# Kernel tuning notes

Hardware: AMD Instinct MI355X
Metric: run time of the kernel (lower is better)

Reference implementation:

```python
import jax, jax.numpy as jnp
import numpy as np

IN_FEATURES = 4096
OUT_FEATURES = 4096
BLOCK_SIZE = 64
P = 0.1          # fraction of blocks kept
N_TOKENS = 8192


def setup_inputs() -> dict:
    key = jax.random.key(0)
    k_x, k_w, k_m, k_b = jax.random.split(key, 4)
    x = jax.random.normal(k_x, (N_TOKENS, IN_FEATURES), dtype=jnp.float32)
    # kaiming_uniform_(a=sqrt(5)) on [out, in] -> bound = 1/sqrt(in_features)
    bound = 1.0 / np.sqrt(IN_FEATURES)
    weight = jax.random.uniform(k_w, (OUT_FEATURES, IN_FEATURES), dtype=jnp.float32,
                                minval=-bound, maxval=bound)
    bias = jax.random.uniform(k_b, (OUT_FEATURES,), dtype=jnp.float32,
                              minval=-bound, maxval=bound)
    # Block-structured 0/1 mask: keep each BLOCK_SIZE x BLOCK_SIZE block with prob P
    nb_out, nb_in = OUT_FEATURES // BLOCK_SIZE, IN_FEATURES // BLOCK_SIZE
    block_keep = (jax.random.uniform(k_m, (nb_out, nb_in)) < P).astype(jnp.float32)
    mask = jnp.repeat(jnp.repeat(block_keep, BLOCK_SIZE, axis=0), BLOCK_SIZE, axis=1)
    return {"input": x, "weight": weight, "bias": bias, "mask": mask}


def reference(input, weight, bias, mask):
    # bsr_dense_mm((W*mask).to_sparse_bsr(), x.T).T + bias == x @ (W*mask).T + bias
    masked_w = weight * mask                      # [out, in]
    return input @ masked_w.T + bias              # [N, out]
```

## Files before the change

kernel.cpp:

```cpp
#include <hip/hip_runtime.h>
#include <hip/hip_fp16.h>
#include <cstdint>

#define IN_F   4096
#define OUT_F  4096
#define BS     64
#define NB     64
#define N_TOK  8192
#define TM     256
#define NMT    (N_TOK / TM)

typedef __attribute__((ext_vector_type(8))) _Float16       f16x8;
typedef __attribute__((ext_vector_type(8))) unsigned short u16x8;
typedef __attribute__((ext_vector_type(4))) unsigned short u16x4;
typedef __attribute__((ext_vector_type(4))) float          f32x4;

#define WS_XT_OFF      0ull
#define WS_XT_BYTES    (2048ull * 32768ull)
#define WS_WT_OFF      (WS_XT_OFF + WS_XT_BYTES)
#define WS_WT_BYTES    (4096ull * 8192ull)
#define WS_NEEDED      (WS_WT_OFF + WS_WT_BYTES)

__device__ __forceinline__ unsigned long long mask_ballot(
        const float* __restrict__ mask, int br, int lane) {
    float mv = mask[(size_t)(br * BS) * IN_F + (size_t)lane * BS];
    return __ballot(mv != 0.0f);
}

__device__ __forceinline__ u16x8 pack8(f32x4 a, f32x4 b) {
    u16x8 o;
#pragma unroll
    for (int j = 0; j < 4; ++j) o[j]     = __half_as_ushort(__float2half_rn(a[j]));
#pragma unroll
    for (int j = 0; j < 4; ++j) o[4 + j] = __half_as_ushort(__float2half_rn(b[j]));
    return o;
}

__global__ __launch_bounds__(256, 2)
void convert_all_kernel(const float* __restrict__ x,
                        const float* __restrict__ w,
                        const float* __restrict__ mask,
                        unsigned short* __restrict__ xt,
                        unsigned short* __restrict__ wt) {
    const int b = blockIdx.x;
    if (b < 1024) {
        __shared__ unsigned short tlds[16][8][64];
        const int xcd = b & 7;
        const int mt  = xcd * 4 + ((b >> 3) & 3);
        const int rb  = b >> 5;
        const int t   = threadIdx.x;
        const size_t xrow0 = (size_t)(mt * TM + rb * 8) * IN_F;
        unsigned short* tb = xt + (size_t)(mt * 64) * 16384;

        const int kb_l = t >> 4;
        const int c4k  = t & 15;
        const int slot = c4k >> 1, h0 = (c4k & 1) * 4;

        for (int j = 0; j < 4; ++j) {
            f32x4 v[8];
#pragma unroll
            for (int l = 0; l < 8; ++l)
                v[l] = *(const f32x4*)(x + xrow0 + (size_t)l * IN_F
                                       + j * 1024 + t * 4);
#pragma unroll
            for (int l = 0; l < 8; ++l) {
                u16x4 o;
#pragma unroll
                for (int k2 = 0; k2 < 4; ++k2)
                    o[k2] = __half_as_ushort(__float2half_rn(v[l][k2]));
                *(u16x4*)&tlds[kb_l][l][((slot ^ l) << 3) + h0] = o;
            }
            __syncthreads();
#pragma unroll
            for (int l = 0; l < 4; ++l) {
                int wid = l * 256 + t;
                int kk = wid >> 6, e = wid & 63;
                int row = e >> 3, s8 = e & 7;
                u16x8 vv = *(const u16x8*)&tlds[kk][row][s8 * 8];
                unsigned short* tile = tb + (size_t)(j * 16 + kk) * 16384;
                *(u16x8*)&tile[(rb * 8 + row) * 64 + s8 * 8] = vv;
            }
            __syncthreads();
        }
    } else {
        const int wb   = b - 1024;
        const int br   = wb >> 6, si = wb & 63;
        const int lane = threadIdx.x & 63;
        unsigned long long ball = mask_ballot(mask, br, lane);
        if (si >= __popcll(ball)) return;
        bool fl = ((ball >> lane) & 1ull) &&
                  (__popcll(ball & ((1ull << lane) - 1ull)) == si);
        unsigned long long m2 = __ballot(fl);
        const int kb = __ffsll(m2) - 1;
        unsigned short* tile = wt + (size_t)(br * NB + si) * 4096;

        f32x4 va[2], vb[2];
#pragma unroll
        for (int l = 0; l < 2; ++l) {
            int g   = threadIdx.x + l * 256;
            int row = g >> 3, slot2 = g & 7;
            const f32x4* src = (const f32x4*)(w + (size_t)(br * BS + row) * IN_F
                                              + kb * BS + slot2 * 8);
            va[l] = src[0];
            vb[l] = src[1];
        }
#pragma unroll
        for (int l = 0; l < 2; ++l) {
            int g   = threadIdx.x + l * 256;
            int row = g >> 3, slot2 = g & 7;
            *(u16x8*)&tile[row * 64 + ((slot2 ^ (row & 7)) << 3)] = pack8(va[l], vb[l]);
        }
    }
}

__device__ __forceinline__ void gll16(const void* g, void* l) {
    __builtin_amdgcn_global_load_lds(
        (const __attribute__((address_space(1))) unsigned int*)g,
        (__attribute__((address_space(3))) unsigned int*)l, 16, 0, 0);
}

__global__ __launch_bounds__(256, 2)
void bsr_mfma5_kernel(const unsigned short* __restrict__ xt,
                      const unsigned short* __restrict__ wt,
                      const float* __restrict__ bias,
                      const float* __restrict__ mask,
                      float* __restrict__ out) {
    __shared__ unsigned short xs[2][TM * BS];
    __shared__ unsigned short wsb[2][BS * BS];

    const int b     = blockIdx.x;
    const int xcd   = b & 7;
    const int j     = b >> 3;
    const int phase = j >> 7;
    const int idx   = j & 127;
    const int br    = idx >> 1;
    const int mt    = xcd * 4 + phase * 2 + (idx & 1);

    const int tid  = threadIdx.x;
    const int lane = tid & 63;
    const int wv   = tid >> 6;
    const int fr   = lane & 15;
    const int kg   = lane >> 4;

    unsigned long long ball = mask_ballot(mask, br, lane);
    const int cnt = __popcll(ball);

    f32x4 acc[4][4];
#pragma unroll
    for (int a = 0; a < 4; ++a)
#pragma unroll
        for (int c = 0; c < 4; ++c) acc[a][c] = (f32x4)0.0f;

    const char* xbase = (const char*)xt;
    const char* wbase = (const char*)wt;

    auto stage = [&](int kb, int si, int bb) {
        const char* xg = xbase + ((size_t)(mt * 64 + kb) << 15);
        const char* wg = wbase + ((size_t)(br * 64 + si) << 13);
        const int bx = wv * 8192;
#pragma unroll
        for (int q = 0; q < 8; ++q)
            gll16(xg + bx + q * 1024 + lane * 16, (char*)xs[bb] + bx + q * 1024);
        const int bw = wv * 2048;
#pragma unroll
        for (int q = 0; q < 2; ++q)
            gll16(wg + bw + q * 1024 + lane * 16, (char*)wsb[bb] + bw + q * 1024);
    };

    unsigned long long rem = ball;
    int cur = 0;
    if (cnt > 0) {
        int kb0 = __ffsll(rem) - 1;
        rem &= rem - 1;
        stage(kb0, 0, 0);
    }
    __syncthreads();

    for (int si = 0; si < cnt; ++si) {
        if (si + 1 < cnt) {
            int kbn = __ffsll(rem) - 1;
            rem &= rem - 1;
            stage(kbn, si + 1, cur ^ 1);
        }

#pragma unroll
        for (int ks = 0; ks < 2; ++ks) {
            f16x8 a[4], bfr[4];
#pragma unroll
            for (int mr = 0; mr < 4; ++mr) {
                int row = wv * 64 + mr * 16 + fr;
                a[mr] = *(const f16x8*)&xs[cur][row * 64 + (((ks * 4 + kg) ^ (row & 7)) << 3)];
            }
#pragma unroll
            for (int nr = 0; nr < 4; ++nr) {
                int row = nr * 16 + fr;
                bfr[nr] = *(const f16x8*)&wsb[cur][row * 64 + (((ks * 4 + kg) ^ (row & 7)) << 3)];
            }
#pragma unroll
            for (int mr = 0; mr < 4; ++mr)
#pragma unroll
                for (int nr = 0; nr < 4; ++nr)
                    acc[mr][nr] = __builtin_amdgcn_mfma_f32_16x16x32_f16(
                        a[mr], bfr[nr], acc[mr][nr], 0, 0, 0);
        }
        __syncthreads();
        cur ^= 1;
    }

    const int mbase = mt * TM;
    const int obase = br * BS;
#pragma unroll
    for (int nr = 0; nr < 4; ++nr) {
        float bv = bias[obase + nr * 16 + fr];
#pragma unroll
        for (int mr = 0; mr < 4; ++mr) {
#pragma unroll
            for (int r = 0; r < 4; ++r) {
                int m = mbase + wv * 64 + mr * 16 + kg * 4 + r;
                out[(size_t)m * OUT_F + obase + nr * 16 + fr] = acc[mr][nr][r] + bv;
            }
        }
    }
}

__global__ __launch_bounds__(256, 3)
void bsr_fused_kernel(const float* __restrict__ x,
                      const float* __restrict__ w,
                      const float* __restrict__ bias,
                      const float* __restrict__ mask,
                      float* __restrict__ out) {
    __shared__ unsigned short xs[128 * BS];
    __shared__ unsigned short wsb[BS * BS];

    const int mt   = blockIdx.x;
    const int br   = blockIdx.y;
    const int tid  = threadIdx.x;
    const int lane = tid & 63;
    const int wv   = tid >> 6;
    const int fr   = lane & 15;
    const int kg   = lane >> 4;

    const int mbase = mt * 128;
    const int obase = br * BS;

    unsigned long long ball = mask_ballot(mask, br, lane);
    const int cnt = __popcll(ball);
    unsigned long long rem = ball;

    f32x4 acc[2][4];
#pragma unroll
    for (int a = 0; a < 2; ++a)
#pragma unroll
        for (int c = 0; c < 4; ++c) acc[a][c] = (f32x4)0.0f;

    for (int si = 0; si < cnt; ++si) {
        const int kb = __ffsll(rem) - 1;
        rem &= rem - 1;
        const int kbase = kb * BS;
#pragma unroll
        for (int l = 0; l < 4; ++l) {
            int g = tid + l * 256;
            int row = g >> 3, slot = g & 7;
            const f32x4* src = (const f32x4*)(x + (size_t)(mbase + row) * IN_F + kbase + slot * 8);
            *(u16x8*)&xs[row * BS + ((slot ^ (row & 7)) << 3)] = pack8(src[0], src[1]);
        }
#pragma unroll
        for (int l = 0; l < 2; ++l) {
            int g = tid + l * 256;
            int row = g >> 3, slot = g & 7;
            const f32x4* src = (const f32x4*)(w + (size_t)(obase + row) * IN_F + kbase + slot * 8);
            *(u16x8*)&wsb[row * BS + ((slot ^ (row & 7)) << 3)] = pack8(src[0], src[1]);
        }
        __syncthreads();
#pragma unroll
        for (int ks = 0; ks < 2; ++ks) {
            f16x8 a[2], bfr[4];
#pragma unroll
            for (int mr = 0; mr < 2; ++mr) {
                int row = wv * 32 + mr * 16 + fr;
                a[mr] = *(const f16x8*)&xs[row * BS + (((ks * 4 + kg) ^ (row & 7)) << 3)];
            }
#pragma unroll
            for (int nr = 0; nr < 4; ++nr) {
                int row = nr * 16 + fr;
                bfr[nr] = *(const f16x8*)&wsb[row * BS + (((ks * 4 + kg) ^ (row & 7)) << 3)];
            }
#pragma unroll
            for (int mr = 0; mr < 2; ++mr)
#pragma unroll
                for (int nr = 0; nr < 4; ++nr)
                    acc[mr][nr] = __builtin_amdgcn_mfma_f32_16x16x32_f16(
                        a[mr], bfr[nr], acc[mr][nr], 0, 0, 0);
        }
        __syncthreads();
    }

#pragma unroll
    for (int nr = 0; nr < 4; ++nr) {
        float bv = bias[obase + nr * 16 + fr];
#pragma unroll
        for (int mr = 0; mr < 2; ++mr) {
#pragma unroll
            for (int r = 0; r < 4; ++r) {
                int m = mbase + wv * 32 + mr * 16 + kg * 4 + r;
                out[(size_t)m * OUT_F + obase + nr * 16 + fr] = acc[mr][nr][r] + bv;
            }
        }
    }
}

extern "C" void kernel_launch(void* const* d_in, const int* in_sizes, int n_in,
                              void* d_out, int out_size, void* d_ws, size_t ws_size,
                              hipStream_t stream) {
    const float* x    = (const float*)d_in[0];
    const float* w    = (const float*)d_in[1];
    const float* bias = (const float*)d_in[2];
    const float* mask = (const float*)d_in[3];
    float* out = (float*)d_out;

    if (ws_size >= WS_NEEDED) {
        unsigned short* xt = (unsigned short*)((char*)d_ws + WS_XT_OFF);
        unsigned short* wt = (unsigned short*)((char*)d_ws + WS_WT_OFF);
        convert_all_kernel<<<1024 + NB * NB, 256, 0, stream>>>(x, w, mask, xt, wt);
        bsr_mfma5_kernel<<<NMT * NB, 256, 0, stream>>>(xt, wt, bias, mask, out);
    } else {
        dim3 grid(N_TOK / 128, NB);
        bsr_fused_kernel<<<grid, 256, 0, stream>>>(x, w, bias, mask, out);
    }
}
```

Baseline: 138.0 us.

## Fuse weight fp16 conversion into BSR matmul and pad x tile stride

Stops pre-converting the masked weight blocks into a separate fp16 workspace. The matmul kernel now loads fp32 weight blocks straight into registers, overlapping that with the MFMA work, and packs them to fp16 in LDS after compute. The x-tile stride in the workspace is padded from 32768 to 33792 bytes, likely to avoid channel or bank aliasing. Each weight block is now re-read from fp32 memory by all 32 M-tiles instead of once, adding global traffic and register pressure to the main loop.

```diff
diff --git a/kernel.cpp b/kernel.cpp
--- a/kernel.cpp
+++ b/kernel.cpp
@@ -10,16 +10,17 @@
 #define TM     256
 #define NMT    (N_TOK / TM)
 
+#define XT_STRIDE_B    33792ull
+#define XT_STRIDE_U16  16896
+
 typedef __attribute__((ext_vector_type(8))) _Float16       f16x8;
 typedef __attribute__((ext_vector_type(8))) unsigned short u16x8;
 typedef __attribute__((ext_vector_type(4))) unsigned short u16x4;
 typedef __attribute__((ext_vector_type(4))) float          f32x4;
 
 #define WS_XT_OFF      0ull
-#define WS_XT_BYTES    (2048ull * 32768ull)
-#define WS_WT_OFF      (WS_XT_OFF + WS_XT_BYTES)
-#define WS_WT_BYTES    (4096ull * 8192ull)
-#define WS_NEEDED      (WS_WT_OFF + WS_WT_BYTES)
+#define WS_XT_BYTES    (2048ull * XT_STRIDE_B)
+#define WS_NEEDED      WS_XT_BYTES
 
 __device__ __forceinline__ unsigned long long mask_ballot(
         const float* __restrict__ mask, int br, int lane) {
@@ -37,79 +38,46 @@
 }
 
 __global__ __launch_bounds__(256, 2)
-void convert_all_kernel(const float* __restrict__ x,
-                        const float* __restrict__ w,
-                        const float* __restrict__ mask,
-                        unsigned short* __restrict__ xt,
-                        unsigned short* __restrict__ wt) {
-    const int b = blockIdx.x;
-    if (b < 1024) {
-        __shared__ unsigned short tlds[16][8][64];
-        const int xcd = b & 7;
-        const int mt  = xcd * 4 + ((b >> 3) & 3);
-        const int rb  = b >> 5;
-        const int t   = threadIdx.x;
-        const size_t xrow0 = (size_t)(mt * TM + rb * 8) * IN_F;
-        unsigned short* tb = xt + (size_t)(mt * 64) * 16384;
-
-        const int kb_l = t >> 4;
-        const int c4k  = t & 15;
-        const int slot = c4k >> 1, h0 = (c4k & 1) * 4;
-
-        for (int j = 0; j < 4; ++j) {
-            f32x4 v[8];
-#pragma unroll
-            for (int l = 0; l < 8; ++l)
-                v[l] = *(const f32x4*)(x + xrow0 + (size_t)l * IN_F
-                                       + j * 1024 + t * 4);
-#pragma unroll
-            for (int l = 0; l < 8; ++l) {
-                u16x4 o;
-#pragma unroll
-                for (int k2 = 0; k2 < 4; ++k2)
-                    o[k2] = __half_as_ushort(__float2half_rn(v[l][k2]));
-                *(u16x4*)&tlds[kb_l][l][((slot ^ l) << 3) + h0] = o;
-            }
-            __syncthreads();
-#pragma unroll
-            for (int l = 0; l < 4; ++l) {
-                int wid = l * 256 + t;
-                int kk = wid >> 6, e = wid & 63;
-                int row = e >> 3, s8 = e & 7;
-                u16x8 vv = *(const u16x8*)&tlds[kk][row][s8 * 8];
-                unsigned short* tile = tb + (size_t)(j * 16 + kk) * 16384;
-                *(u16x8*)&tile[(rb * 8 + row) * 64 + s8 * 8] = vv;
-            }
-            __syncthreads();
-        }
-    } else {
-        const int wb   = b - 1024;
-        const int br   = wb >> 6, si = wb & 63;
-        const int lane = threadIdx.x & 63;
-        unsigned long long ball = mask_ballot(mask, br, lane);
-        if (si >= __popcll(ball)) return;
-        bool fl = ((ball >> lane) & 1ull) &&
-                  (__popcll(ball & ((1ull << lane) - 1ull)) == si);
-        unsigned long long m2 = __ballot(fl);
-        const int kb = __ffsll(m2) - 1;
-        unsigned short* tile = wt + (size_t)(br * NB + si) * 4096;
-
-        f32x4 va[2], vb[2];
-#pragma unroll
-        for (int l = 0; l < 2; ++l) {
-            int g   = threadIdx.x + l * 256;
-            int row = g >> 3, slot2 = g & 7;
-            const f32x4* src = (const f32x4*)(w + (size_t)(br * BS + row) * IN_F
-                                              + kb * BS + slot2 * 8);
-            va[l] = src[0];
-            vb[l] = src[1];
-        }
-#pragma unroll
-        for (int l = 0; l < 2; ++l) {
-            int g   = threadIdx.x + l * 256;
-            int row = g >> 3, slot2 = g & 7;
-            *(u16x8*)&tile[row * 64 + ((slot2 ^ (row & 7)) << 3)] = pack8(va[l], vb[l]);
-        }
+void convert_x_kernel(const float* __restrict__ x,
+                      unsigned short* __restrict__ xt) {
+    __shared__ unsigned short tlds[16][8][64];
+    const int b   = blockIdx.x;
+    const int xcd = b & 7;
+    const int mt  = xcd * 4 + ((b >> 3) & 3);
+    const int rb  = b >> 5;
+    const int t   = threadIdx.x;
+    const size_t xrow0 = (size_t)(mt * TM + rb * 8) * IN_F;
+    unsigned short* tb = xt + (size_t)(mt * 64) * XT_STRIDE_U16;
+
+    const int kb_l = t >> 4;
+    const int c4k  = t & 15;
+    const int slot = c4k >> 1, h0 = (c4k & 1) * 4;
+
+    for (int j = 0; j < 4; ++j) {
+        f32x4 v[8];
+#pragma unroll
+        for (int l = 0; l < 8; ++l)
+            v[l] = *(const f32x4*)(x + xrow0 + (size_t)l * IN_F
+                                   + j * 1024 + t * 4);
+#pragma unroll
+        for (int l = 0; l < 8; ++l) {
+            u16x4 o;
+#pragma unroll
+            for (int k2 = 0; k2 < 4; ++k2)
+                o[k2] = __half_as_ushort(__float2half_rn(v[l][k2]));
+            *(u16x4*)&tlds[kb_l][l][((slot ^ l) << 3) + h0] = o;
+        }
+        __syncthreads();
+#pragma unroll
+        for (int l = 0; l < 4; ++l) {
+            int wid = l * 256 + t;
+            int kk = wid >> 6, e = wid & 63;
+            int row = e >> 3, s8 = e & 7;
+            u16x8 vv = *(const u16x8*)&tlds[kk][row][s8 * 8];
+            unsigned short* tile = tb + (size_t)(j * 16 + kk) * XT_STRIDE_U16;
+            *(u16x8*)&tile[(rb * 8 + row) * 64 + s8 * 8] = vv;
+        }
+        __syncthreads();
     }
 }
 
@@ -120,8 +88,8 @@
 }
 
 __global__ __launch_bounds__(256, 2)
-void bsr_mfma5_kernel(const unsigned short* __restrict__ xt,
-                      const unsigned short* __restrict__ wt,
+void bsr_mfma8_kernel(const unsigned short* __restrict__ xt,
+                      const float* __restrict__ w,
                       const float* __restrict__ bias,
                       const float* __restrict__ mask,
                       float* __restrict__ out) {
@@ -152,19 +120,33 @@
         for (int c = 0; c < 4; ++c) acc[a][c] = (f32x4)0.0f;
 
     const char* xbase = (const char*)xt;
-    const char* wbase = (const char*)wt;
-
-    auto stage = [&](int kb, int si, int bb) {
-        const char* xg = xbase + ((size_t)(mt * 64 + kb) << 15);
-        const char* wg = wbase + ((size_t)(br * 64 + si) << 13);
+    const int obase = br * BS;
+
+    auto stageA = [&](int kb, int bb) {
+        const char* xg = xbase + (size_t)(mt * 64 + kb) * XT_STRIDE_B;
         const int bx = wv * 8192;
 #pragma unroll
         for (int q = 0; q < 8; ++q)
             gll16(xg + bx + q * 1024 + lane * 16, (char*)xs[bb] + bx + q * 1024);
-        const int bw = wv * 2048;
-#pragma unroll
-        for (int q = 0; q < 2; ++q)
-            gll16(wg + bw + q * 1024 + lane * 16, (char*)wsb[bb] + bw + q * 1024);
+    };
+    f32x4 rw[2][2];
+    auto loadW = [&](int kb) {
+#pragma unroll
+        for (int l = 0; l < 2; ++l) {
+            int g = tid + l * 256, row = g >> 3, slot = g & 7;
+            const f32x4* src = (const f32x4*)(w + (size_t)(obase + row) * IN_F
+                                              + kb * BS + slot * 8);
+            rw[l][0] = src[0];
+            rw[l][1] = src[1];
+        }
+    };
+    auto commitW = [&](int bb) {
+#pragma unroll
+        for (int l = 0; l < 2; ++l) {
+            int g = tid + l * 256, row = g >> 3, slot = g & 7;
+            *(u16x8*)&wsb[bb][row * 64 + ((slot ^ (row & 7)) << 3)]
+                = pack8(rw[l][0], rw[l][1]);
+        }
     };
 
     unsigned long long rem = ball;
@@ -172,15 +154,19 @@
     if (cnt > 0) {
         int kb0 = __ffsll(rem) - 1;
         rem &= rem - 1;
-        stage(kb0, 0, 0);
+        loadW(kb0);
+        stageA(kb0, 0);
+        commitW(0);
     }
     __syncthreads();
 
     for (int si = 0; si < cnt; ++si) {
-        if (si + 1 < cnt) {
+        const bool more = (si + 1 < cnt);
+        if (more) {
             int kbn = __ffsll(rem) - 1;
             rem &= rem - 1;
-            stage(kbn, si + 1, cur ^ 1);
+            loadW(kbn);
+            stageA(kbn, cur ^ 1);
         }
 
 #pragma unroll
@@ -203,12 +189,12 @@
                     acc[mr][nr] = __builtin_amdgcn_mfma_f32_16x16x32_f16(
                         a[mr], bfr[nr], acc[mr][nr], 0, 0, 0);
         }
+        if (more) commitW(cur ^ 1);
         __syncthreads();
         cur ^= 1;
     }
 
     const int mbase = mt * TM;
-    const int obase = br * BS;
 #pragma unroll
     for (int nr = 0; nr < 4; ++nr) {
         float bv = bias[obase + nr * 16 + fr];
@@ -320,9 +306,8 @@
 
     if (ws_size >= WS_NEEDED) {
         unsigned short* xt = (unsigned short*)((char*)d_ws + WS_XT_OFF);
-        unsigned short* wt = (unsigned short*)((char*)d_ws + WS_WT_OFF);
-        convert_all_kernel<<<1024 + NB * NB, 256, 0, stream>>>(x, w, mask, xt, wt);
-        bsr_mfma5_kernel<<<NMT * NB, 256, 0, stream>>>(xt, wt, bias, mask, out);
+        convert_x_kernel<<<1024, 256, 0, stream>>>(x, xt);
+        bsr_mfma8_kernel<<<NMT * NB, 256, 0, stream>>>(xt, w, bias, mask, out);
     } else {
         dim3 grid(N_TOK / 128, NB);
         bsr_fused_kernel<<<grid, 256, 0, stream>>>(x, w, bias, mask, out);
```

Result: no change. 139.4 us (+1.0%).
